# Kernel tuning notes

Hardware: AMD Instinct MI355X
Metric: run time of the kernel (lower is better)

Reference implementation:

```python
import jax, jax.numpy as jnp
import numpy as np

RECALL_THRESHOLD = 0.3
LAMBDA_PAUC = 0.5
NUM_CLASSES = 128
LABEL_SMOOTHING = 0.1
N_SAMPLES = 131072


def setup_inputs() -> dict:
    key = jax.random.key(0)
    k1, k2 = jax.random.split(key)
    predictions = jax.random.normal(k1, (N_SAMPLES, NUM_CLASSES), dtype=jnp.float32)
    targets = jax.random.randint(k2, (N_SAMPLES,), 0, NUM_CLASSES)
    return {"predictions": predictions, "targets": targets}


def _macro_pauc(probs, targets):
    """Vectorized (over classes) partial AUC at max_fpr = 1 - recall_threshold.

    Equivalent to the per-class torch loop: descending argsort of scores,
    cumsum TP/FP, clip the ROC curve at max_fpr with linear interpolation of
    the crossing segment, trapezoidal integration, macro-average over classes
    that have at least one positive.
    """
    N, K = probs.shape
    order = jnp.argsort(-probs, axis=0)                      # [N, K] descending per class
    t_sorted = (targets[order] == jnp.arange(K)[None, :]).astype(probs.dtype)  # [N, K]
    tps = jnp.cumsum(t_sorted, axis=0)                        # [N, K]
    fps = jnp.cumsum(1.0 - t_sorted, axis=0)                  # [N, K]
    tpr = tps / jnp.maximum(tps[-1], 1.0)
    fpr = fps / jnp.maximum(fps[-1], 1.0)

    max_fpr = 1.0 - RECALL_THRESHOLD
    # Clip fpr at max_fpr; segments fully beyond the cut get delta == 0 so
    # their tpr value is irrelevant. The crossing segment's right endpoint is
    # replaced by the linearly interpolated tpr at max_fpr (matches torch's
    # slope-based interpolation with the same 1e-8 guard).
    fpr_c = jnp.minimum(fpr, max_fpr)
    slope = (tpr[1:] - tpr[:-1]) / (fpr[1:] - fpr[:-1] + 1e-8)
    tpr_interp = tpr[:-1] + slope * (max_fpr - fpr[:-1])
    tpr_next = jnp.where(fpr[1:] <= max_fpr, tpr[1:], tpr_interp)
    delta = fpr_c[1:] - fpr_c[:-1]                            # [N-1, K]
    pauc_c = jnp.sum(delta * 0.5 * (tpr_next + tpr[:-1]), axis=0)  # [K]

    valid = (tps[-1] > 0).astype(probs.dtype)                 # macro: skip empty classes
    return jnp.sum(pauc_c * valid) / jnp.maximum(jnp.sum(valid), 1.0)


def reference(predictions, targets):
    logp = jax.nn.log_softmax(predictions, axis=1)
    probs = jnp.exp(logp)
    # CrossEntropyLoss with label smoothing (mean reduction, no class weights):
    # loss_i = (1-eps) * nll_i + eps * mean_c(-log p_ic)
    nll = -jnp.take_along_axis(logp, targets[:, None], axis=1)[:, 0]
    smooth = -jnp.mean(logp, axis=1)
    ce_loss = jnp.mean((1.0 - LABEL_SMOOTHING) * nll + LABEL_SMOOTHING * smooth)

    # torch.tensor(pauc) in the original detaches pAUC from the graph.
    pauc = jax.lax.stop_gradient(_macro_pauc(probs, targets))
    pauc_loss = 1.0 - pauc ** 2
    return (1.0 - LAMBDA_PAUC) * ce_loss + LAMBDA_PAUC * pauc_loss
```

## Files before the change

### kernel.cpp

```cpp
#include <hip/hip_runtime.h>
#include <math.h>

#define N_SAMPLES 131072
#define NUM_CLASSES 128
#define NB 64
#define MAX_FPR 0.7f
#define NBLK 512
#define ROWS_PER_BLK 256
#define HP 33
#define PART_WORDS 6144

typedef unsigned int u32;

__device__ __forceinline__ int bin_of(float x, float off ) {
    int b = (int)__fmaf_rn(x, 4.0f, off);
    return min(max(b, 0), NB - 1);
}

__global__ __launch_bounds__(1024, 8) void fused_kernel(
    const float* __restrict__ pred, const int* __restrict__ tgt,
    u32* __restrict__ part,
    float* __restrict__ ceArr,
    u32* __restrict__ doneCtr)
{
    __shared__ u32 hA[NUM_CLASSES * HP];
    __shared__ u32 hP[NUM_CLASSES * HP];
    __shared__ float wsum[16];

    const int tid  = threadIdx.x;
    const int w    = tid >> 6;
    const int lane = tid & 63;
    const int j    = lane & 15;
    const int rs   = lane >> 4;

    for (int i = tid; i < NUM_CLASSES * HP; i += 1024) { hA[i] = 0u; hP[i] = 0u; }
    if (blockIdx.x == 0 && tid == 0) *doneCtr = 0u;
    __syncthreads();

    const int rowBase = blockIdx.x * ROWS_PER_BLK + w * 4 + rs;
    float acc_lse = 0.0f, acc_xt = 0.0f, acc_sx = 0.0f;

    const float* r0p = pred + (size_t)rowBase * 128;
    float4 a0 = *(const float4*)(r0p + j * 4);
    float4 a1 = *(const float4*)(r0p + 64 + j * 4);
    int    ta = tgt[rowBase];
    const float* r1p = r0p + (size_t)64 * 128;
    float4 c0 = *(const float4*)(r1p + j * 4);
    float4 c1 = *(const float4*)(r1p + 64 + j * 4);
    int    tb = tgt[rowBase + 64];

    #pragma unroll
    for (int p = 0; p < 4; p++) {
        float4 n0, n1; int tn = 0;
        if (p < 2) {
            const float* rn = pred + (size_t)(rowBase + (p + 2) * 64) * 128;
            n0 = *(const float4*)(rn + j * 4);
            n1 = *(const float4*)(rn + 64 + j * 4);
            tn = tgt[rowBase + (p + 2) * 64];
        }

        float e = __expf(a0.x) + __expf(a0.y) + __expf(a0.z) + __expf(a0.w)
                + __expf(a1.x) + __expf(a1.y) + __expf(a1.z) + __expf(a1.w);
        #pragma unroll
        for (int o = 1; o < 16; o <<= 1) e += __shfl_xor(e, o);
        const float lse = __logf(e);
        const float off = (14.0f - lse) * 4.0f;

        const float xv[8] = {a0.x, a0.y, a0.z, a0.w, a1.x, a1.y, a1.z, a1.w};
        #pragma unroll
        for (int q = 0; q < 8; q++) {
            const int c = (q < 4) ? (j * 4 + q) : (64 + j * 4 + (q - 4));
            const int b = bin_of(xv[q], off);
            const int word = ((b >> 1) + j) & 31;
            atomicAdd(&hA[c * HP + word], (b & 1) ? 65536u : 1u);
        }

        acc_sx  += (xv[0] + xv[1] + xv[2] + xv[3])
                 + (xv[4] + xv[5] + xv[6] + xv[7]);
        acc_lse += lse * 0.0625f;

        {
            const int t = ta;
            float xt; bool hit = false;
            if ((t >> 2) == j)                        { xt = xv[t & 3];       hit = true; }
            else if (t >= 64 && ((t - 64) >> 2) == j) { xt = xv[4 + (t & 3)]; hit = true; }
            if (hit) {
                acc_xt += xt;
                const int bp = bin_of(xt, off);
                atomicAdd(&hP[t * HP + (((bp >> 1) + j) & 31)],
                          (bp & 1) ? 65536u : 1u);
            }
        }

        a0 = c0; a1 = c1; ta = tb;
        c0 = n0; c1 = n1; tb = tn;
    }

    float ce = acc_lse - 0.9f * acc_xt - (0.1f / 128.0f) * acc_sx;
    #pragma unroll
    for (int o = 32; o; o >>= 1) ce += __shfl_xor(ce, o);
    if (lane == 0) wsum[w] = ce;
    __syncthreads();
    if (tid == 0) {
        float s = 0.0f;
        #pragma unroll
        for (int i = 0; i < 16; i++) s += wsum[i];
        ceArr[blockIdx.x] = s;
    }

    u32* outp = part + (size_t)blockIdx.x * PART_WORDS;
    for (int i = tid; i < 4096; i += 1024) {
        const int c = i >> 5, bw = i & 31;
        const int src = c * HP + ((bw + ((c >> 2) & 15)) & 31);
        outp[i] = hA[src];
    }
    for (int i = tid; i < 2048; i += 1024) {
        const int c  = i >> 4, w4 = i & 15;
        const int jc = (c >> 2) & 15;
        const u32 lo = hP[c * HP + (((2 * w4)     + jc) & 31)];
        const u32 hi = hP[c * HP + (((2 * w4 + 1) + jc) & 31)];
        const u32 b0 = min(lo & 0xffffu, 255u);
        const u32 b1 = min(lo >> 16,     255u);
        const u32 b2 = min(hi & 0xffffu, 255u);
        const u32 b3 = min(hi >> 16,     255u);
        outp[4096 + i] = b0 | (b1 << 8) | (b2 << 16) | (b3 << 24);
    }
}

__global__ __launch_bounds__(1024) void pauc_reduce(
    const u32* __restrict__ part, const float* __restrict__ ceArr,
    float* __restrict__ paucArr, float* __restrict__ validArr,
    u32* __restrict__ doneCtr, float* __restrict__ out)
{
    __shared__ u32 aB[NB], pB[NB];

    const int k  = blockIdx.x;
    const int t  = threadIdx.x;
    const int w  = t & 31;
    const int sl = t >> 5;

    if (t < NB) { aB[t] = 0u; pB[t] = 0u; }
    __syncthreads();

    u32 alo = 0u, ahi = 0u, plo = 0u, phi = 0u;
    const u32* baseA = part + (size_t)(sl * 16) * PART_WORDS + k * 32 + w;
    const u32* baseP = part + (size_t)(sl * 16) * PART_WORDS + 4096 + k * 16 + (w >> 1);
    const int  psh   = 16 * (w & 1);
    #pragma unroll 8
    for (int b = 0; b < 16; b++) {
        const u32 qa = baseA[(size_t)b * PART_WORDS];
        const u32 qp = baseP[(size_t)b * PART_WORDS];
        alo += qa & 0xffffu;            ahi += qa >> 16;
        plo += (qp >> psh) & 0xffu;     phi += (qp >> (psh + 8)) & 0xffu;
    }
    atomicAdd(&aB[2 * w], alo); atomicAdd(&aB[2 * w + 1], ahi);
    atomicAdd(&pB[2 * w], plo); atomicAdd(&pB[2 * w + 1], phi);
    __syncthreads();

    if (t < 64) {
        const int l = t;
        const u32 a = aB[63 - l];
        const u32 p = pB[63 - l];

        u32 ia = a, ip = p;
        #pragma unroll
        for (int o = 1; o < 64; o <<= 1) {
            const u32 tA = __shfl_up(ia, o);
            const u32 tP = __shfl_up(ip, o);
            if (l >= o) { ia += tA; ip += tP; }
        }
        const u32 P = __shfl(ip, 63);
        const u32 T = __shfl(ia, 63);
        const float Pm = fmaxf((float)P, 1.0f);
        const float Fm = fmaxf((float)(T - P), 1.0f);

        const int cumA = (int)(ia - a), cumP = (int)(ip - p);
        float contrib = 0.0f;
        const int f = (int)a - (int)p;
        if (f > 0) {
            const float fpr0 = (float)(cumA - cumP) / Fm;
            if (fpr0 < MAX_FPR) {
                const float tpr0 = (float)cumP / Pm;
                const float tpr1 = (float)(cumP + (int)p) / Pm;
                const float fpr1 = (float)(cumA - cumP + f) / Fm;
                if (fpr1 <= MAX_FPR) {
                    contrib = (fpr1 - fpr0) * 0.5f * (tpr0 + tpr1);
                } else {
                    const float tfrac = (MAX_FPR - fpr0) / (fpr1 - fpr0);
                    const float tprc  = tpr0 + tfrac * (tpr1 - tpr0);
                    contrib = (MAX_FPR - fpr0) * 0.5f * (tpr0 + tprc);
                }
            }
        }
        #pragma unroll
        for (int o = 32; o; o >>= 1) contrib += __shfl_xor(contrib, o);

        int isLast = 0;
        if (l == 0) {
            paucArr[k]  = (P > 0u) ? contrib : 0.0f;
            validArr[k] = (P > 0u) ? 1.0f : 0.0f;
            __threadfence();
            const u32 tk = atomicAdd(doneCtr, 1u);
            isLast = (tk == NUM_CLASSES - 1);
        }
        isLast = __shfl(isLast, 0);

        if (isLast) {
            float s1 = 0.0f, s2 = 0.0f, s3 = 0.0f;
            #pragma unroll
            for (int i = l; i < NUM_CLASSES; i += 64) {
                s1 += __hip_atomic_load(paucArr + i,  __ATOMIC_RELAXED,
                                        __HIP_MEMORY_SCOPE_AGENT);
                s2 += __hip_atomic_load(validArr + i, __ATOMIC_RELAXED,
                                        __HIP_MEMORY_SCOPE_AGENT);
            }
            #pragma unroll
            for (int i = l; i < NBLK; i += 64) s3 += ceArr[i];
            #pragma unroll
            for (int o = 32; o; o >>= 1) {
                s1 += __shfl_xor(s1, o);
                s2 += __shfl_xor(s2, o);
                s3 += __shfl_xor(s3, o);
            }
            if (l == 0) {
                const float cem  = s3 * (1.0f / (float)N_SAMPLES);
                const float pauc = s1 / fmaxf(s2, 1.0f);
                out[0] = 0.5f * cem + 0.5f * (1.0f - pauc * pauc);
            }
        }
    }
}

extern "C" void kernel_launch(void* const* d_in, const int* in_sizes, int n_in,
                              void* d_out, int out_size, void* d_ws, size_t ws_size,
                              hipStream_t stream)
{
    const float* pred = (const float*)d_in[0];
    const int*   tgt  = (const int*)d_in[1];

    char* ws = (char*)d_ws;
    u32*   part    = (u32*)ws;
    float* ceArr   = (float*)(ws + 12582912);
    float* paucArr = (float*)(ws + 12582912 + 2048);
    float* validArr= (float*)(ws + 12582912 + 2560);
    u32*   doneCtr = (u32*)  (ws + 12582912 + 3072);

    fused_kernel<<<NBLK, 1024, 0, stream>>>(pred, tgt, part, ceArr, doneCtr);
    pauc_reduce<<<NUM_CLASSES, 1024, 0, stream>>>(part, ceArr, paucArr, validArr,
                                                  doneCtr, (float*)d_out);
}
```

Before: 102.9 us.

## Split per-class pAUC reduction across two blocks with last-arriver merge

The reduce kernel now launches two blocks per class, each summing half of the 512 per-block histogram partials. Each block publishes its half-histogram to global memory, and a per-class atomic counter elects the second arriving block. That block adds the other half and computes the class's pAUC. The goal is more parallelism and shorter per-block load chains in the reduction. The cost is an extra global store/load round trip, more control counters to reset, and reliance on cross-block memory fences.

New measurement: 107.4 us. 4.4% more time.

```diff
diff --git a/kernel.cpp b/kernel.cpp
--- a/kernel.cpp
+++ b/kernel.cpp
@@ -21,7 +21,7 @@
     const float* __restrict__ pred, const int* __restrict__ tgt,
     u32* __restrict__ part,
     float* __restrict__ ceArr,
-    u32* __restrict__ doneCtr)
+    u32* __restrict__ ctrl)
 {
     __shared__ u32 hA[NUM_CLASSES * HP];
     __shared__ u32 hP[NUM_CLASSES * HP];
@@ -34,7 +34,7 @@
     const int rs   = lane >> 4;
 
     for (int i = tid; i < NUM_CLASSES * HP; i += 1024) { hA[i] = 0u; hP[i] = 0u; }
-    if (blockIdx.x == 0 && tid == 0) *doneCtr = 0u;
+    if (blockIdx.x == 0 && tid < 129) ctrl[tid] = 0u;
     __syncthreads();
 
     const int rowBase = blockIdx.x * ROWS_PER_BLK + w * 4 + rs;
@@ -130,11 +130,15 @@
 __global__ __launch_bounds__(1024) void pauc_reduce(
     const u32* __restrict__ part, const float* __restrict__ ceArr,
     float* __restrict__ paucArr, float* __restrict__ validArr,
-    u32* __restrict__ doneCtr, float* __restrict__ out)
+    u32* __restrict__ ctrl,
+    u32* __restrict__ gHalf,
+    float* __restrict__ out)
 {
     __shared__ u32 aB[NB], pB[NB];
-
-    const int k  = blockIdx.x;
+    __shared__ u32 role;
+
+    const int k  = blockIdx.x & 127;
+    const int h  = blockIdx.x >> 7;
     const int t  = threadIdx.x;
     const int w  = t & 31;
     const int sl = t >> 5;
@@ -143,11 +147,11 @@
     __syncthreads();
 
     u32 alo = 0u, ahi = 0u, plo = 0u, phi = 0u;
-    const u32* baseA = part + (size_t)(sl * 16) * PART_WORDS + k * 32 + w;
-    const u32* baseP = part + (size_t)(sl * 16) * PART_WORDS + 4096 + k * 16 + (w >> 1);
+    const u32* baseA = part + (size_t)(h * 256 + sl * 8) * PART_WORDS + k * 32 + w;
+    const u32* baseP = part + (size_t)(h * 256 + sl * 8) * PART_WORDS + 4096 + k * 16 + (w >> 1);
     const int  psh   = 16 * (w & 1);
-    #pragma unroll 8
-    for (int b = 0; b < 16; b++) {
+    #pragma unroll
+    for (int b = 0; b < 8; b++) {
         const u32 qa = baseA[(size_t)b * PART_WORDS];
         const u32 qp = baseP[(size_t)b * PART_WORDS];
         alo += qa & 0xffffu;            ahi += qa >> 16;
@@ -157,10 +161,28 @@
     atomicAdd(&pB[2 * w], plo); atomicAdd(&pB[2 * w + 1], phi);
     __syncthreads();
 
+    if (t < 2 * NB) {
+        const u32 v = (t < NB) ? aB[t] : pB[t - NB];
+        __hip_atomic_store(&gHalf[(size_t)((h << 7) + k) * 128 + t], v,
+                           __ATOMIC_RELAXED, __HIP_MEMORY_SCOPE_AGENT);
+    }
+    __syncthreads();
+    if (t == 0) {
+        __threadfence();
+        role = atomicAdd(&ctrl[1 + k], 1u);
+    }
+    __syncthreads();
+    if (role == 0u) return;
+
     if (t < 64) {
         const int l = t;
-        const u32 a = aB[63 - l];
-        const u32 p = pB[63 - l];
+        const u32* oth = gHalf + (size_t)(((h ^ 1) << 7) + k) * 128;
+        const u32 a = aB[63 - l] +
+            __hip_atomic_load(&oth[63 - l],      __ATOMIC_RELAXED,
+                              __HIP_MEMORY_SCOPE_AGENT);
+        const u32 p = pB[63 - l] +
+            __hip_atomic_load(&oth[64 + 63 - l], __ATOMIC_RELAXED,
+                              __HIP_MEMORY_SCOPE_AGENT);
 
         u32 ia = a, ip = p;
         #pragma unroll
@@ -200,7 +222,7 @@
             paucArr[k]  = (P > 0u) ? contrib : 0.0f;
             validArr[k] = (P > 0u) ? 1.0f : 0.0f;
             __threadfence();
-            const u32 tk = atomicAdd(doneCtr, 1u);
+            const u32 tk = atomicAdd(&ctrl[0], 1u);
             isLast = (tk == NUM_CLASSES - 1);
         }
         isLast = __shfl(isLast, 0);
@@ -243,9 +265,11 @@
     float* ceArr   = (float*)(ws + 12582912);
     float* paucArr = (float*)(ws + 12582912 + 2048);
     float* validArr= (float*)(ws + 12582912 + 2560);
-    u32*   doneCtr = (u32*)  (ws + 12582912 + 3072);
-
-    fused_kernel<<<NBLK, 1024, 0, stream>>>(pred, tgt, part, ceArr, doneCtr);
-    pauc_reduce<<<NUM_CLASSES, 1024, 0, stream>>>(part, ceArr, paucArr, validArr,
-                                                  doneCtr, (float*)d_out);
-}
+    u32*   ctrl    = (u32*)  (ws + 12582912 + 3072);
+    u32*   gHalf   = (u32*)  (ws + 12582912 + 4096);
+
+    fused_kernel<<<NBLK, 1024, 0, stream>>>(pred, tgt, part, ceArr, ctrl);
+    pauc_reduce<<<2 * NUM_CLASSES, 1024, 0, stream>>>(part, ceArr, paucArr,
+                                                      validArr, ctrl, gHalf,
+                                                      (float*)d_out);
+}
```
